# Kernel tuning notes

Measured on AMD Instinct MI355X. Metric: run time of the kernel, lower is better.

## Reference

```python
import jax, jax.numpy as jnp
import numpy as np
from jax import lax

N = 50000      # nodes
E = 1600000    # edges
F = 128        # input features
G = 32         # gnn_hidden_dim
H = 50         # lstm hidden_dim
SEQ = 10       # sequence_length


def setup_inputs() -> dict:
    key = jax.random.key(0)
    ks = jax.random.split(key, 12)
    s = 0.05
    return {
        "x": jax.random.normal(ks[0], (N, F), jnp.float32),
        "W_gcn": jax.random.normal(ks[1], (F, G), jnp.float32) * s,
        "b_gcn": jnp.zeros((G,), jnp.float32),
        "w_ih0": jax.random.normal(ks[2], (4 * H, G), jnp.float32) * s,
        "w_hh0": jax.random.normal(ks[3], (4 * H, H), jnp.float32) * s,
        "b_ih0": jnp.zeros((4 * H,), jnp.float32),
        "b_hh0": jnp.zeros((4 * H,), jnp.float32),
        "w_ih1": jax.random.normal(ks[4], (4 * H, H), jnp.float32) * s,
        "w_hh1": jax.random.normal(ks[5], (4 * H, H), jnp.float32) * s,
        "b_ih1": jnp.zeros((4 * H,), jnp.float32),
        "b_hh1": jnp.zeros((4 * H,), jnp.float32),
        "fc_w": jax.random.normal(ks[6], (1, H), jnp.float32) * s,
        "fc_b": jnp.zeros((1,), jnp.float32),
        "edge_index": jax.random.randint(ks[7], (2, E), 0, N, dtype=jnp.int64),
        "seq_len": SEQ,
    }


def gcn_conv(x, edge_index, W, b):
    # PyG GCNConv: add self-loops, symmetric deg^{-1/2} normalization,
    # linear transform, gather-scale-scatter aggregation at target nodes.
    n = x.shape[0]
    loop = jnp.arange(n, dtype=edge_index.dtype)
    src = jnp.concatenate([edge_index[0], loop])  # message sources j
    dst = jnp.concatenate([edge_index[1], loop])  # aggregation targets i
    deg = jax.ops.segment_sum(jnp.ones_like(dst, dtype=x.dtype), dst,
                              num_segments=n)
    dinv = jnp.where(deg > 0, lax.rsqrt(jnp.maximum(deg, 1.0)), 0.0)
    norm = dinv[src] * dinv[dst]                       # [E+N]
    h = x @ W                                          # [N, G]
    msg = h[src] * norm[:, None]                       # gather + scale
    out = jax.ops.segment_sum(msg, dst, num_segments=n)
    return out + b


def lstm_layer(x_proj, w_hh, b_hh):
    # x_proj: [T, B, 4H] precomputed input projections (i,f,g,o gate order).
    T, B, H4 = x_proj.shape
    Hd = H4 // 4
    h0 = jnp.zeros((B, Hd), x_proj.dtype)
    c0 = jnp.zeros((B, Hd), x_proj.dtype)

    def step(carry, xp):
        h, c = carry
        gates = xp + h @ w_hh.T + b_hh
        i, f, g, o = jnp.split(gates, 4, axis=-1)
        i, f, o = jax.nn.sigmoid(i), jax.nn.sigmoid(f), jax.nn.sigmoid(o)
        g = jnp.tanh(g)
        c = f * c + i * g
        h = o * jnp.tanh(c)
        return (h, c), h

    (h, c), ys = lax.scan(step, (h0, c0), x_proj)
    return ys, h


def reference(x, W_gcn, b_gcn, w_ih0, w_hh0, b_ih0, b_hh0,
              w_ih1, w_hh1, b_ih1, b_hh1, fc_w, fc_b,
              edge_index, seq_len):
    gnn_out = gcn_conv(x, edge_index, W_gcn, b_gcn)        # [N, G]
    # lstm_in = gnn_out repeated seq_len times -> input projection is
    # identical per step; compute once and broadcast (same math).
    p0 = gnn_out @ w_ih0.T + b_ih0                         # [N, 4H]
    x_proj0 = jnp.broadcast_to(p0, (seq_len,) + p0.shape)  # [T, N, 4H]
    ys0, _ = lstm_layer(x_proj0, w_hh0, b_hh0)             # [T, N, H]
    x_proj1 = ys0 @ w_ih1.T + b_ih1                        # [T, N, 4H]
    _, hn1 = lstm_layer(x_proj1, w_hh1, b_hh1)             # [N, H]
    return hn1 @ fc_w.T + fc_b                             # [N, 1]
```

## Files before the change

kernel.cpp:

```cpp
#include <hip/hip_runtime.h>
#include <hip/hip_bf16.h>

typedef __attribute__((ext_vector_type(8))) short short8;
typedef __attribute__((ext_vector_type(4))) float f32x4;

#define L2E 1.442695041f
#define SCAN_B 256

__device__ __forceinline__ short f2bf(float f) {
  union { __hip_bfloat16 b; short s; } u;
  u.b = __float2bfloat16(f);
  return u.s;
}

__device__ __forceinline__ float ldh(const float* p, size_t i) { return p[i]; }
__device__ __forceinline__ float ldh(const __hip_bfloat16* p, size_t i) {
  return __bfloat162float(p[i]);
}
__device__ __forceinline__ void sth(float* p, size_t i, float v) { p[i] = v; }
__device__ __forceinline__ void sth(__hip_bfloat16* p, size_t i, float v) {
  p[i] = __float2bfloat16(v);
}

__device__ __forceinline__ short8 load_gfrag(const float* g, size_t base) {
  const float4* gp = (const float4*)(g + base);
  float4 a = gp[0], b = gp[1];
  short8 t;
  t[0]=f2bf(a.x); t[1]=f2bf(a.y); t[2]=f2bf(a.z); t[3]=f2bf(a.w);
  t[4]=f2bf(b.x); t[5]=f2bf(b.y); t[6]=f2bf(b.z); t[7]=f2bf(b.w);
  return t;
}
__device__ __forceinline__ short8 load_gfrag(const __hip_bfloat16* g, size_t base) {
  return *(const short8*)(g + base);
}

#define OFF_WIH0 0
#define OFF_WHH0 13312
#define OFF_WIH1 39936
#define OFF_WHH1 66560
#define OFF_B0   93184
#define OFF_B1   94016
#define OFF_FCW  94848
#define IMG_BYTES 95056

__global__ void k_detect(const int* __restrict__ ei, int* __restrict__ flag) {
  if (threadIdx.x == 0 && blockIdx.x == 0) {
    int odd_nz = 0, even_nz = 0;
    for (int i = 0; i < 128; ++i) {
      odd_nz |= (ei[2 * i + 1] != 0);
      even_nz |= (ei[2 * i] != 0);
    }
    *flag = (even_nz && !odd_nz) ? 1 : 0;
  }
}


__global__ void k_count(const int* __restrict__ ei, int E,
                        const int* __restrict__ flag, int* __restrict__ cnt) {
  int e = blockIdx.x * blockDim.x + threadIdx.x;
  if (e < E) {
    int d = (*flag) ? ei[2 * (E + e)] : ei[E + e];
    atomicAdd(&cnt[d], 1);
  }
}

__global__ void k_convert(const int* __restrict__ ei, int E,
                          const int* __restrict__ flag,
                          unsigned int* __restrict__ ed, int* __restrict__ cnt) {
  int e = blockIdx.x * blockDim.x + threadIdx.x;
  if (e < E) {
    int is64 = *flag;
    int s = is64 ? ei[2 * e] : ei[e];
    int d = is64 ? ei[2 * (E + e)] : ei[E + e];
    ed[e] = (unsigned int)s | ((unsigned int)d << 16);
    atomicAdd(&cnt[d], 1);
  }
}

__global__ void k_dinv(const int* __restrict__ cnt, float* __restrict__ dinv, int N) {
  int i = blockIdx.x * blockDim.x + threadIdx.x;
  if (i < N) dinv[i] = rsqrtf((float)cnt[i] + 1.0f);
}

__global__ __launch_bounds__(256) void k_scanA(const int* __restrict__ cnt,
                                               float* __restrict__ dinv,
                                               int* __restrict__ bsum, int N) {
  __shared__ int red[256];
  int b = blockIdx.x, t = threadIdx.x;
  int chunk = (N + SCAN_B - 1) / SCAN_B;
  int lo = b * chunk, hi = min(lo + chunk, N);
  int s = 0;
  for (int i = lo + t; i < hi; i += 256) {
    int c = cnt[i];
    dinv[i] = rsqrtf((float)c + 1.0f);
    s += c;
  }
  red[t] = s;
  __syncthreads();
  for (int o = 128; o > 0; o >>= 1) {
    if (t < o) red[t] += red[t + o];
    __syncthreads();
  }
  if (t == 0) bsum[b] = red[0];
}

__global__ __launch_bounds__(256) void k_scanB(int* __restrict__ a,
                                               const int* __restrict__ bsum,
                                               int N) {
  __shared__ int sh[256];
  int b = blockIdx.x, t = threadIdx.x;
  int chunk = (N + SCAN_B - 1) / SCAN_B;
  int lo = b * chunk, hi = min(lo + chunk, N);
  sh[t] = bsum[t];
  __syncthreads();
  for (int o = 1; o < 256; o <<= 1) {
    int u = (t >= o) ? sh[t - o] : 0;
    __syncthreads();
    sh[t] += u;
    __syncthreads();
  }
  int carry = (b == 0) ? 0 : sh[b - 1];
  __syncthreads();
  for (int i0 = lo; i0 < hi; i0 += 256) {
    int i = i0 + t;
    int c = (i < hi) ? a[i] : 0;
    sh[t] = c;
    __syncthreads();
    for (int o = 1; o < 256; o <<= 1) {
      int u = (t >= o) ? sh[t - o] : 0;
      __syncthreads();
      sh[t] += u;
      __syncthreads();
    }
    if (i < hi) a[i] = carry + sh[t] - c;
    carry += sh[255];
    __syncthreads();
  }
}

__global__ void k_fill_p(const unsigned int* __restrict__ ed, int E,
                         int* __restrict__ rowst,
                         unsigned short* __restrict__ csr, int lo, int hi) {
  int e = blockIdx.x * blockDim.x + threadIdx.x;
  if (e < E) {
    unsigned int v = ed[e];
    int d = (int)(v >> 16);
    if (d >= lo && d < hi) {
      int p = atomicAdd(&rowst[d], 1);
      csr[p] = (unsigned short)(v & 0xFFFFu);
    }
  }
}

template <typename CT>
__global__ void k_fill(const int* __restrict__ ei, int E,
                       const int* __restrict__ flag,
                       int* __restrict__ rowst, CT* __restrict__ csr,
                       int lo, int hi) {
  int e = blockIdx.x * blockDim.x + threadIdx.x;
  if (e < E) {
    int is64 = *flag;
    int d = is64 ? ei[2 * (E + e)] : ei[E + e];
    if (d >= lo && d < hi) {
      int s = is64 ? ei[2 * e] : ei[e];
      int p = atomicAdd(&rowst[d], 1);
      csr[p] = (CT)s;
    }
  }
}

template <typename HT>
__global__ __launch_bounds__(256) void k_hs(const float* __restrict__ x,
                                            const float* __restrict__ Wg,
                                            const float* __restrict__ dinv,
                                            HT* __restrict__ hs, int N) {
  __shared__ __align__(16) float xt[64][132];
  __shared__ __align__(16) float Wl[128][32];
  int tid = threadIdx.x;
  int nb = blockIdx.x * 64;
  for (int i = tid; i < 4096; i += 256) Wl[i >> 5][i & 31] = Wg[i];
  const float4* xv = (const float4*)x;
  for (int i = tid; i < 2048; i += 256) {
    int r = i >> 5, c = i & 31;
    float4 v = make_float4(0.f, 0.f, 0.f, 0.f);
    if (nb + r < N) v = xv[(size_t)(nb + r) * 32 + c];
    *(float4*)&xt[r][c * 4] = v;
  }
  __syncthreads();
  int nl = tid >> 2, gq = (tid & 3) * 8;
  float a[8];
#pragma unroll
  for (int j = 0; j < 8; ++j) a[j] = 0.f;
  for (int k = 0; k < 128; ++k) {
    float xk = xt[nl][k];
#pragma unroll
    for (int j = 0; j < 8; ++j) a[j] += xk * Wl[k][gq + j];
  }
  int n = nb + nl;
  if (n < N) {
    float d = dinv[n];
#pragma unroll
    for (int j = 0; j < 8; ++j) sth(hs, (size_t)n * 32 + gq + j, a[j] * d);
  }
}

template <typename HT, typename GT, typename CT>
__global__ void k_gather(const CT* __restrict__ csr, const int* __restrict__ rowst,
                         const HT* __restrict__ hs, const float* __restrict__ dinv,
                         const float* __restrict__ bg, GT* __restrict__ gout,
                         int N) {
  int w = (blockIdx.x * blockDim.x + threadIdx.x) >> 6;
  if (w >= N) return;
  int l = threadIdx.x & 63;
  int g = l & 31, j = l >> 5;
  int end = rowst[w];
  int start = (w == 0) ? 0 : rowst[w - 1];
  int deg = end - start;
  int dmax = min(deg, 64);
  int idx = (l < deg) ? (int)csr[start + l] : 0;
  float acc = 0.0f;
#pragma unroll 1
  for (int base = 0; base < 64; base += 16) {
    if (base >= dmax) break;
#pragma unroll
    for (int i = 0; i < 8; ++i) {
      int e = base + 2 * i + j;
      int src = __shfl(idx, e);
      float v = ldh(hs, (size_t)src * 32 + g);
      acc += (e < dmax) ? v : 0.0f;
    }
  }
  for (int k = start + 64 + j; k < end; k += 2)
    acc += ldh(hs, (size_t)csr[k] * 32 + g);
  acc += __shfl_xor(acc, 32);
  if (j == 0) {
    float v = (acc + ldh(hs, (size_t)w * 32 + g)) * dinv[w] + bg[g];
    sth(gout, (size_t)w * 32 + g, v);
  }
}

template <typename HT>
__global__ void k_scatter(const int* __restrict__ ei, int E,
                          const int* __restrict__ flag,
                          const HT* __restrict__ hs, float* __restrict__ gout) {
  long long gid = (long long)blockIdx.x * blockDim.x + threadIdx.x;
  int e = (int)(gid >> 3), part = (int)(gid & 7);
  if (e >= E) return;
  int is64 = *flag;
  int s = is64 ? ei[2 * e] : ei[e];
  int d = is64 ? ei[2 * (E + e)] : ei[E + e];
  int b = part * 4;
  float* gp = gout + (size_t)d * 32 + b;
  size_t hp = (size_t)s * 32 + b;
  atomicAdd(gp + 0, ldh(hs, hp + 0));
  atomicAdd(gp + 1, ldh(hs, hp + 1));
  atomicAdd(gp + 2, ldh(hs, hp + 2));
  atomicAdd(gp + 3, ldh(hs, hp + 3));
}
template <typename HT>
__global__ void k_finish(const HT* __restrict__ hs, const float* __restrict__ dinv,
                         const float* __restrict__ bg, float* __restrict__ gout,
                         int N) {
  int gid = blockIdx.x * blockDim.x + threadIdx.x;
  if (gid < N * 32) {
    int n = gid >> 5, g = gid & 31;
    gout[gid] = (gout[gid] + ldh(hs, (size_t)gid)) * dinv[n] + bg[g];
  }
}

__global__ void k_prep(const float* __restrict__ wih0, const float* __restrict__ whh0,
                       const float* __restrict__ wih1, const float* __restrict__ whh1,
                       const float* __restrict__ bih0, const float* __restrict__ bhh0,
                       const float* __restrict__ bih1, const float* __restrict__ bhh1,
                       const float* __restrict__ fcw, unsigned char* __restrict__ img) {
  int gid = blockIdx.x * blockDim.x + threadIdx.x;
  int nthr = gridDim.x * blockDim.x;
  {
    short* W = (short*)(img + OFF_WIH0);
    for (int i = gid; i < 208 * 32; i += nthr) {
      int row = i >> 5, k = i & 31, u = row >> 2, q = row & 3;
      float sc = (q == 2) ? 2.0f * L2E : -L2E;
      float v = (u < 50) ? wih0[(q * 50 + u) * 32 + k] * sc : 0.0f;
      W[row * 32 + (k ^ ((row & 3) << 3))] = f2bf(v);
    }
  }
  {
    short* W = (short*)(img + OFF_WHH0);
    for (int i = gid; i < 208 * 64; i += nthr) {
      int row = i >> 6, k = i & 63, u = row >> 2, q = row & 3;
      float sc = (q == 2) ? 2.0f * L2E : -L2E;
      float v = (u < 50 && k < 50) ? whh0[(q * 50 + u) * 50 + k] * sc : 0.0f;
      W[row * 64 + (k ^ ((row & 7) << 3))] = f2bf(v);
    }
  }
  {
    short* W = (short*)(img + OFF_WIH1);
    for (int i = gid; i < 208 * 64; i += nthr) {
      int row = i >> 6, k = i & 63, u = row >> 2, q = row & 3;
      float sc = (q == 2) ? 2.0f * L2E : -L2E;
      float v = (u < 50 && k < 50) ? wih1[(q * 50 + u) * 50 + k] * sc : 0.0f;
      W[row * 64 + (k ^ ((row & 7) << 3))] = f2bf(v);
    }
  }
  {
    short* W = (short*)(img + OFF_WHH1);
    for (int i = gid; i < 208 * 64; i += nthr) {
      int row = i >> 6, k = i & 63, u = row >> 2, q = row & 3;
      float sc = (q == 2) ? 2.0f * L2E : -L2E;
      float v = (u < 50 && k < 50) ? whh1[(q * 50 + u) * 50 + k] * sc : 0.0f;
      W[row * 64 + (k ^ ((row & 7) << 3))] = f2bf(v);
    }
  }
  {
    float* B = (float*)(img + OFF_B0);
    for (int i = gid; i < 208; i += nthr) {
      int u = i >> 2, q = i & 3;
      float sc = (q == 2) ? 2.0f * L2E : -L2E;
      B[i] = (u < 50) ? (bih0[q * 50 + u] + bhh0[q * 50 + u]) * sc : 0.0f;
    }
  }
  {
    float* B = (float*)(img + OFF_B1);
    for (int i = gid; i < 208; i += nthr) {
      int u = i >> 2, q = i & 3;
      float sc = (q == 2) ? 2.0f * L2E : -L2E;
      B[i] = (u < 50) ? (bih1[q * 50 + u] + bhh1[q * 50 + u]) * sc : 0.0f;
    }
  }
  {
    float* F = (float*)(img + OFF_FCW);
    for (int i = gid; i < 52; i += nthr) F[i] = (i < 50) ? fcw[i] : 0.0f;
  }
}

__device__ __forceinline__ float gate_update(const f32x4& acc, float& cp) {
  float ei = __builtin_amdgcn_exp2f(acc[0]);
  float ef = __builtin_amdgcn_exp2f(acc[1]);
  float eo = __builtin_amdgcn_exp2f(acc[3]);
  float iv = __builtin_amdgcn_rcpf(1.0f + ei);
  float fv = __builtin_amdgcn_rcpf(1.0f + ef);
  float ov = __builtin_amdgcn_rcpf(1.0f + eo);
  float eg = __builtin_amdgcn_exp2f(fminf(acc[2], 80.0f));
  float gv = (eg - 1.0f) * __builtin_amdgcn_rcpf(eg + 1.0f);
  float c = fv * cp + iv * gv;
  cp = c;
  float Ec = __builtin_amdgcn_exp2f(c * (2.0f * L2E));
  float th = (Ec - 1.0f) * __builtin_amdgcn_rcpf(Ec + 1.0f);
  return ov * th;
}

template <typename GT>
__global__ __launch_bounds__(512, 2) void k_lstm(const GT* __restrict__ gout,
    const unsigned char* __restrict__ img, const float* __restrict__ fcb_p,
    float* __restrict__ out, int N) {
  __shared__ __align__(16) unsigned char smem[160592];
  const int tid = threadIdx.x;
  {
    const uint4* s = (const uint4*)img;
    uint4* d = (uint4*)smem;
    for (int i = tid; i < IMG_BYTES / 16; i += 512) d[i] = s[i];
  }
  __syncthreads();
  const int lane = tid & 63, wid = tid >> 6;
  const int l15 = lane & 15, l4 = lane >> 4;
  const int swz7 = (l15 & 7) << 3, swz3 = (l15 & 3) << 3;
  const int node0 = blockIdx.x * 256 + wid * 32;

  const short* WIH0 = (const short*)(smem + OFF_WIH0);
  const short* WHH0 = (const short*)(smem + OFF_WHH0);
  const short* WIH1 = (const short*)(smem + OFF_WIH1);
  const short* WHH1 = (const short*)(smem + OFF_WHH1);
  const float* B0   = (const float*)(smem + OFF_B0);
  const float* B1   = (const float*)(smem + OFF_B1);
  const float* FCW  = (const float*)(smem + OFF_FCW);
  short* h0st = (short*)(smem + IMG_BYTES + wid * 8192);
  short* h1st = h0st + 2048;

  {
    uint4 z; z.x = z.y = z.z = z.w = 0u;
    uint4* p = (uint4*)h0st;
    for (int i = lane; i < 512; i += 64) p[i] = z;
  }

  f32x4 p0r[13][2];
  {
    short8 gfrag[2];
#pragma unroll
    for (int v = 0; v < 2; ++v) {
      int node = node0 + v * 16 + l15;
      short8 t = {0, 0, 0, 0, 0, 0, 0, 0};
      if (node < N) t = load_gfrag(gout, (size_t)node * 32 + l4 * 8);
      gfrag[v] = t;
    }
#pragma unroll
    for (int t = 0; t < 13; ++t) {
      short8 w = *(const short8*)(WIH0 + (16 * t + l15) * 32 + ((l4 * 8) ^ swz3));
      f32x4 bv = *(const f32x4*)(B0 + t * 16 + l4 * 4);
#pragma unroll
      for (int v = 0; v < 2; ++v)
        p0r[t][v] = __builtin_amdgcn_mfma_f32_16x16x32_bf16(w, gfrag[v], bv, 0, 0, 0);
    }
  }

  float c0[13][2], c1[13][2];
#pragma unroll
  for (int t = 0; t < 13; ++t) { c0[t][0]=0.f; c0[t][1]=0.f; c1[t][0]=0.f; c1[t][1]=0.f; }
  float facc[2] = {0.f, 0.f};

#pragma unroll 1
  for (int s = 0; s < 10; ++s) {
    short8 h0f[2][2], h1f[2][2];
#pragma unroll
    for (int c = 0; c < 2; ++c)
#pragma unroll
      for (int v = 0; v < 2; ++v) {
        int nl = v * 16 + l15;
        h0f[c][v] = *(const short8*)(h0st + nl * 64 + ((c * 32 + l4 * 8) ^ swz7));
        h1f[c][v] = *(const short8*)(h1st + nl * 64 + ((c * 32 + l4 * 8) ^ swz7));
      }
#pragma unroll
    for (int t = 0; t < 13; ++t) {
      int arow = (16 * t + l15);
      short8 ah0 = *(const short8*)(WHH0 + arow * 64 + ((l4 * 8) ^ swz7));
      short8 ah1 = *(const short8*)(WHH0 + arow * 64 + ((32 + l4 * 8) ^ swz7));
#pragma unroll
      for (int v = 0; v < 2; ++v) {
        f32x4 acc = p0r[t][v];
        acc = __builtin_amdgcn_mfma_f32_16x16x32_bf16(ah0, h0f[0][v], acc, 0, 0, 0);
        acc = __builtin_amdgcn_mfma_f32_16x16x32_bf16(ah1, h0f[1][v], acc, 0, 0, 0);
        float h = gate_update(acc, c0[t][v]);
        h0st[(v * 16 + l15) * 64 + ((4 * t + l4) ^ swz7)] = f2bf(h);
      }
    }
    short8 h0nf[2][2];
#pragma unroll
    for (int c = 0; c < 2; ++c)
#pragma unroll
      for (int v = 0; v < 2; ++v) {
        int nl = v * 16 + l15;
        h0nf[c][v] = *(const short8*)(h0st + nl * 64 + ((c * 32 + l4 * 8) ^ swz7));
      }
#pragma unroll
    for (int t = 0; t < 13; ++t) {
      f32x4 bv = *(const f32x4*)(B1 + t * 16 + l4 * 4);
      int arow = (16 * t + l15);
      short8 ai0 = *(const short8*)(WIH1 + arow * 64 + ((l4 * 8) ^ swz7));
      short8 ai1 = *(const short8*)(WIH1 + arow * 64 + ((32 + l4 * 8) ^ swz7));
      short8 ah0 = *(const short8*)(WHH1 + arow * 64 + ((l4 * 8) ^ swz7));
      short8 ah1 = *(const short8*)(WHH1 + arow * 64 + ((32 + l4 * 8) ^ swz7));
#pragma unroll
      for (int v = 0; v < 2; ++v) {
        f32x4 acc = bv;
        acc = __builtin_amdgcn_mfma_f32_16x16x32_bf16(ai0, h0nf[0][v], acc, 0, 0, 0);
        acc = __builtin_amdgcn_mfma_f32_16x16x32_bf16(ai1, h0nf[1][v], acc, 0, 0, 0);
        acc = __builtin_amdgcn_mfma_f32_16x16x32_bf16(ah0, h1f[0][v], acc, 0, 0, 0);
        acc = __builtin_amdgcn_mfma_f32_16x16x32_bf16(ah1, h1f[1][v], acc, 0, 0, 0);
        float h = gate_update(acc, c1[t][v]);
        h1st[(v * 16 + l15) * 64 + ((4 * t + l4) ^ swz7)] = f2bf(h);
        if (s == 9) {
          int u = 4 * t + l4;
          facc[v] += FCW[u] * h;
        }
      }
    }
  }
  float fcb = fcb_p[0];
#pragma unroll
  for (int v = 0; v < 2; ++v) {
    float r = facc[v];
    r += __shfl_xor(r, 16);
    r += __shfl_xor(r, 32);
    int node = node0 + v * 16 + l15;
    if (l4 == 0 && node < N) out[node] = r + fcb;
  }
}

extern "C" void kernel_launch(void* const* d_in, const int* in_sizes, int n_in,
                              void* d_out, int out_size, void* d_ws, size_t ws_size,
                              hipStream_t stream) {
  const float* x    = (const float*)d_in[0];
  const float* Wg   = (const float*)d_in[1];
  const float* bg   = (const float*)d_in[2];
  const float* wih0 = (const float*)d_in[3];
  const float* whh0 = (const float*)d_in[4];
  const float* bih0 = (const float*)d_in[5];
  const float* bhh0 = (const float*)d_in[6];
  const float* wih1 = (const float*)d_in[7];
  const float* whh1 = (const float*)d_in[8];
  const float* bih1 = (const float*)d_in[9];
  const float* bhh1 = (const float*)d_in[10];
  const float* fcw  = (const float*)d_in[11];
  const float* fcb  = (const float*)d_in[12];
  const int*   edge = (const int*)d_in[13];
  int N = in_sizes[0] / 128;
  int E = in_sizes[13] / 2;

  char* ws = (char*)d_ws;
  size_t off = 0;
  auto take = [&](size_t b) {
    size_t o = off;
    off = (off + b + 255) & ~(size_t)255;
    return o;
  };
  int*   rowst = (int*)(ws + take((size_t)N * 4));
  float* dinv  = (float*)(ws + take((size_t)N * 4));
  int*   flag  = (int*)(ws + take(256));
  unsigned char* wimg = (unsigned char*)(ws + take(IMG_BYTES));
  size_t base = off;

  const int NP = 4;
  int span = (N + NP - 1) / NP;
  bool canU16 = (N <= 65535) && (E <= 100000000);

  size_t csr_b  = ((size_t)E * 2 + 255) & ~(size_t)255;
  size_t hsb    = ((size_t)N * 64 + 255) & ~(size_t)255;
  size_t reg2_b = (size_t)E * 4 > 2 * hsb ? (size_t)E * 4 : 2 * hsb;
  size_t needP  = base + csr_b + reg2_b;
  size_t needA = base + (((size_t)N * 128 + 255) & ~(size_t)255)
               + (((size_t)E * 4 + 255) & ~(size_t)255)
               + ((size_t)N * 128);

  hipMemsetAsync(rowst, 0, (size_t)N * 4, stream);
  k_detect<<<1, 1, 0, stream>>>(edge, flag);
  k_prep<<<52, 256, 0, stream>>>(wih0, whh0, wih1, whh1, bih0, bhh0, bih1, bhh1,
                                 fcw, wimg);

  if (ws_size >= needA) {
    float* gout = (float*)(ws + take((size_t)N * 128));
    int*   csr  = (int*)(ws + take((size_t)E * 4));
    float* hs   = (float*)(ws + take((size_t)N * 128));
    int*   bsum = (int*)csr;
    k_count<<<(E + 255) / 256, 256, 0, stream>>>(edge, E, flag, rowst);
    k_scanA<<<SCAN_B, 256, 0, stream>>>(rowst, dinv, bsum, N);
    k_scanB<<<SCAN_B, 256, 0, stream>>>(rowst, bsum, N);
    k_hs<float><<<(N + 63) / 64, 256, 0, stream>>>(x, Wg, dinv, hs, N);
    for (int p = 0; p < NP; ++p) {
      int lo = p * span, hi = min(lo + span, N);
      if (lo >= hi) break;
      k_fill<int><<<(E + 255) / 256, 256, 0, stream>>>(edge, E, flag, rowst,
                                                       csr, lo, hi);
    }
    k_gather<float, float, int><<<(N + 3) / 4, 256, 0, stream>>>(
        csr, rowst, hs, dinv, bg, gout, N);
    k_lstm<float><<<(N + 255) / 256, 512, 0, stream>>>(gout, wimg, fcb,
                                                       (float*)d_out, N);
  } else if (canU16 && ws_size >= needP) {
    unsigned short* csr = (unsigned short*)(ws + take(csr_b));
    char* reg2 = ws + take(reg2_b);
    unsigned int*   ed   = (unsigned int*)reg2;
    __hip_bfloat16* hs   = (__hip_bfloat16*)reg2;
    __hip_bfloat16* gout = (__hip_bfloat16*)(reg2 + hsb);
    int* bsum = (int*)csr;

    k_convert<<<(E + 255) / 256, 256, 0, stream>>>(edge, E, flag, ed, rowst);
    k_scanA<<<SCAN_B, 256, 0, stream>>>(rowst, dinv, bsum, N);
    k_scanB<<<SCAN_B, 256, 0, stream>>>(rowst, bsum, N);
    for (int p = 0; p < NP; ++p) {
      int lo = p * span, hi = min(lo + span, N);
      if (lo >= hi) break;
      k_fill_p<<<(E + 255) / 256, 256, 0, stream>>>(ed, E, rowst, csr, lo, hi);
    }
    k_hs<__hip_bfloat16><<<(N + 63) / 64, 256, 0, stream>>>(x, Wg, dinv, hs, N);
    k_gather<__hip_bfloat16, __hip_bfloat16, unsigned short>
        <<<(N + 3) / 4, 256, 0, stream>>>(csr, rowst, hs, dinv, bg, gout, N);
    k_lstm<__hip_bfloat16><<<(N + 255) / 256, 512, 0, stream>>>(gout, wimg, fcb,
                                                                (float*)d_out, N);
  } else {
    float* gout = (float*)(ws + take((size_t)N * 128));
    __hip_bfloat16* hs = (__hip_bfloat16*)(ws + take((size_t)N * 64));
    hipMemsetAsync(gout, 0, (size_t)N * 128, stream);
    k_count<<<(E + 255) / 256, 256, 0, stream>>>(edge, E, flag, rowst);
    k_dinv<<<(N + 255) / 256, 256, 0, stream>>>(rowst, dinv, N);
    k_hs<__hip_bfloat16><<<(N + 63) / 64, 256, 0, stream>>>(x, Wg, dinv, hs, N);
    int sc_blocks = (int)(((long long)E * 8 + 255) / 256);
    k_scatter<__hip_bfloat16><<<sc_blocks, 256, 0, stream>>>(edge, E, flag, hs, gout);
    k_finish<__hip_bfloat16><<<(N * 32 + 255) / 256, 256, 0, stream>>>(
        hs, dinv, bg, gout, N);
    k_lstm<float><<<(N + 255) / 256, 512, 0, stream>>>(gout, wimg, fcb,
                                                       (float*)d_out, N);
  }
}
```

Measured before the change: 343.7 us.

## Fold memset and dtype detection into other kernels, merge reciprocals, halve fill passes

The rowst memset moves into k_prep, and int64 detection is computed per block inside k_convert, so two launches leave the active path. Gate_update pairs reciprocals so two rcp instructions replace four. The FC dot product now reads h from shared memory once after the loop instead of accumulating on the final step. The number of CSR fill partitions drops from 4 to 2, which means fewer passes over the edges but less locality per pass.

```diff
diff --git a/kernel.cpp b/kernel.cpp
--- a/kernel.cpp
+++ b/kernel.cpp
@@ -11,6 +11,10 @@
   union { __hip_bfloat16 b; short s; } u;
   u.b = __float2bfloat16(f);
   return u.s;
+}
+__device__ __forceinline__ float b2f(short s) {
+  unsigned u = ((unsigned)(unsigned short)s) << 16;
+  return __uint_as_float(u);
 }
 
 __device__ __forceinline__ float ldh(const float* p, size_t i) { return p[i]; }
@@ -41,12 +45,13 @@
 #define OFF_B0   93184
 #define OFF_B1   94016
 #define OFF_FCW  94848
-#define IMG_BYTES 95056
-
-__global__ void k_detect(const int* __restrict__ ei, int* __restrict__ flag) {
+#define IMG_BYTES 95104
+
+__global__ void k_detect(const int* __restrict__ ei, int E, int* __restrict__ flag) {
   if (threadIdx.x == 0 && blockIdx.x == 0) {
     int odd_nz = 0, even_nz = 0;
-    for (int i = 0; i < 128; ++i) {
+    int m = min(128, E);
+    for (int i = 0; i < m; ++i) {
       odd_nz |= (ei[2 * i + 1] != 0);
       even_nz |= (ei[2 * i] != 0);
     }
@@ -65,11 +70,21 @@
 }
 
 __global__ void k_convert(const int* __restrict__ ei, int E,
-                          const int* __restrict__ flag,
                           unsigned int* __restrict__ ed, int* __restrict__ cnt) {
+  __shared__ int sflag;
+  if (threadIdx.x == 0) {
+    int odd_nz = 0, even_nz = 0;
+    int m = min(128, E);
+    for (int i = 0; i < m; ++i) {
+      odd_nz |= (ei[2 * i + 1] != 0);
+      even_nz |= (ei[2 * i] != 0);
+    }
+    sflag = (even_nz && !odd_nz) ? 1 : 0;
+  }
+  __syncthreads();
+  int is64 = sflag;
   int e = blockIdx.x * blockDim.x + threadIdx.x;
   if (e < E) {
-    int is64 = *flag;
     int s = is64 ? ei[2 * e] : ei[e];
     int d = is64 ? ei[2 * (E + e)] : ei[E + e];
     ed[e] = (unsigned int)s | ((unsigned int)d << 16);
@@ -272,9 +287,11 @@
                        const float* __restrict__ wih1, const float* __restrict__ whh1,
                        const float* __restrict__ bih0, const float* __restrict__ bhh0,
                        const float* __restrict__ bih1, const float* __restrict__ bhh1,
-                       const float* __restrict__ fcw, unsigned char* __restrict__ img) {
+                       const float* __restrict__ fcw, unsigned char* __restrict__ img,
+                       int* __restrict__ rowst, int N) {
   int gid = blockIdx.x * blockDim.x + threadIdx.x;
   int nthr = gridDim.x * blockDim.x;
+  for (int i = gid; i < N; i += nthr) rowst[i] = 0;
   {
     short* W = (short*)(img + OFF_WIH0);
     for (int i = gid; i < 208 * 32; i += nthr) {
@@ -329,7 +346,7 @@
   }
   {
     float* F = (float*)(img + OFF_FCW);
-    for (int i = gid; i < 52; i += nthr) F[i] = (i < 50) ? fcw[i] : 0.0f;
+    for (int i = gid; i < 64; i += nthr) F[i] = (i < 50) ? fcw[i] : 0.0f;
   }
 }
 
@@ -337,11 +354,14 @@
   float ei = __builtin_amdgcn_exp2f(acc[0]);
   float ef = __builtin_amdgcn_exp2f(acc[1]);
   float eo = __builtin_amdgcn_exp2f(acc[3]);
-  float iv = __builtin_amdgcn_rcpf(1.0f + ei);
-  float fv = __builtin_amdgcn_rcpf(1.0f + ef);
-  float ov = __builtin_amdgcn_rcpf(1.0f + eo);
   float eg = __builtin_amdgcn_exp2f(fminf(acc[2], 80.0f));
-  float gv = (eg - 1.0f) * __builtin_amdgcn_rcpf(eg + 1.0f);
+  float a = 1.0f + ei, b = 1.0f + ef;
+  float rif = __builtin_amdgcn_rcpf(a * b);
+  float iv = rif * b, fv = rif * a;
+  float o1 = 1.0f + eo, g1 = eg + 1.0f;
+  float rog = __builtin_amdgcn_rcpf(o1 * g1);
+  float ov = rog * g1;
+  float gv = (eg - 1.0f) * (rog * o1);
   float c = fv * cp + iv * gv;
   cp = c;
   float Ec = __builtin_amdgcn_exp2f(c * (2.0f * L2E));
@@ -353,7 +373,7 @@
 __global__ __launch_bounds__(512, 2) void k_lstm(const GT* __restrict__ gout,
     const unsigned char* __restrict__ img, const float* __restrict__ fcb_p,
     float* __restrict__ out, int N) {
-  __shared__ __align__(16) unsigned char smem[160592];
+  __shared__ __align__(16) unsigned char smem[160640];
   const int tid = threadIdx.x;
   {
     const uint4* s = (const uint4*)img;
@@ -405,7 +425,6 @@
   float c0[13][2], c1[13][2];
 #pragma unroll
   for (int t = 0; t < 13; ++t) { c0[t][0]=0.f; c0[t][1]=0.f; c1[t][0]=0.f; c1[t][1]=0.f; }
-  float facc[2] = {0.f, 0.f};
 
 #pragma unroll 1
   for (int s = 0; s < 10; ++s) {
@@ -457,21 +476,25 @@
         acc = __builtin_amdgcn_mfma_f32_16x16x32_bf16(ah1, h1f[1][v], acc, 0, 0, 0);
         float h = gate_update(acc, c1[t][v]);
         h1st[(v * 16 + l15) * 64 + ((4 * t + l4) ^ swz7)] = f2bf(h);
-        if (s == 9) {
-          int u = 4 * t + l4;
-          facc[v] += FCW[u] * h;
-        }
       }
     }
   }
   float fcb = fcb_p[0];
 #pragma unroll
   for (int v = 0; v < 2; ++v) {
-    float r = facc[v];
-    r += __shfl_xor(r, 16);
-    r += __shfl_xor(r, 32);
+    int nl = v * 16 + l15;
+    float facc = 0.f;
+#pragma unroll
+    for (int c = 0; c < 2; ++c) {
+      short8 f = *(const short8*)(h1st + nl * 64 + ((c * 32 + l4 * 8) ^ swz7));
+#pragma unroll
+      for (int j = 0; j < 8; ++j)
+        facc += b2f(f[j]) * FCW[c * 32 + l4 * 8 + j];
+    }
+    facc += __shfl_xor(facc, 16);
+    facc += __shfl_xor(facc, 32);
     int node = node0 + v * 16 + l15;
-    if (l4 == 0 && node < N) out[node] = r + fcb;
+    if (l4 == 0 && node < N) out[node] = facc + fcb;
   }
 }
 
@@ -508,7 +531,7 @@
   unsigned char* wimg = (unsigned char*)(ws + take(IMG_BYTES));
   size_t base = off;
 
-  const int NP = 4;
+  const int NP = 2;
   int span = (N + NP - 1) / NP;
   bool canU16 = (N <= 65535) && (E <= 100000000);
 
@@ -520,16 +543,15 @@
                + (((size_t)E * 4 + 255) & ~(size_t)255)
                + ((size_t)N * 128);
 
-  hipMemsetAsync(rowst, 0, (size_t)N * 4, stream);
-  k_detect<<<1, 1, 0, stream>>>(edge, flag);
   k_prep<<<52, 256, 0, stream>>>(wih0, whh0, wih1, whh1, bih0, bhh0, bih1, bhh1,
-                                 fcw, wimg);
+                                 fcw, wimg, rowst, N);
 
   if (ws_size >= needA) {
     float* gout = (float*)(ws + take((size_t)N * 128));
     int*   csr  = (int*)(ws + take((size_t)E * 4));
     float* hs   = (float*)(ws + take((size_t)N * 128));
     int*   bsum = (int*)csr;
+    k_detect<<<1, 1, 0, stream>>>(edge, E, flag);
     k_count<<<(E + 255) / 256, 256, 0, stream>>>(edge, E, flag, rowst);
     k_scanA<<<SCAN_B, 256, 0, stream>>>(rowst, dinv, bsum, N);
     k_scanB<<<SCAN_B, 256, 0, stream>>>(rowst, bsum, N);
@@ -552,7 +574,7 @@
     __hip_bfloat16* gout = (__hip_bfloat16*)(reg2 + hsb);
     int* bsum = (int*)csr;
 
-    k_convert<<<(E + 255) / 256, 256, 0, stream>>>(edge, E, flag, ed, rowst);
+    k_convert<<<(E + 255) / 256, 256, 0, stream>>>(edge, E, ed, rowst);
     k_scanA<<<SCAN_B, 256, 0, stream>>>(rowst, dinv, bsum, N);
     k_scanB<<<SCAN_B, 256, 0, stream>>>(rowst, bsum, N);
     for (int p = 0; p < NP; ++p) {
@@ -569,6 +591,7 @@
     float* gout = (float*)(ws + take((size_t)N * 128));
     __hip_bfloat16* hs = (__hip_bfloat16*)(ws + take((size_t)N * 64));
     hipMemsetAsync(gout, 0, (size_t)N * 128, stream);
+    k_detect<<<1, 1, 0, stream>>>(edge, E, flag);
     k_count<<<(E + 255) / 256, 256, 0, stream>>>(edge, E, flag, rowst);
     k_dinv<<<(N + 255) / 256, 256, 0, stream>>>(rowst, dinv, N);
     k_hs<__hip_bfloat16><<<(N + 63) / 64, 256, 0, stream>>>(x, Wg, dinv, hs, N);
```

New measurement: 349.9 us. About the same (+1.8%).
